# Performance work log

Measured on AMD Instinct MI355X. Metric: run time of the kernel, lower is better.

## Reference

```python
import jax, jax.numpy as jnp
import numpy as np

D_MODEL = 1024
NUM_HEADS = 16
D_KEY = D_MODEL // NUM_HEADS


def setup_inputs() -> dict:
    key = jax.random.key(0)
    ks = jax.random.split(key, 9)
    s = 1.0 / np.sqrt(D_MODEL)
    inp = {
        "x": jax.random.normal(ks[0], (4, 2048, D_MODEL), dtype=jnp.float32),
        "Wq": jax.random.uniform(ks[1], (D_MODEL, D_MODEL), jnp.float32, -s, s),
        "bq": jax.random.uniform(ks[2], (D_MODEL,), jnp.float32, -s, s),
        "Wk": jax.random.uniform(ks[3], (D_MODEL, D_MODEL), jnp.float32, -s, s),
        "bk": jax.random.uniform(ks[4], (D_MODEL,), jnp.float32, -s, s),
        "Wv": jax.random.uniform(ks[5], (D_MODEL, D_MODEL), jnp.float32, -s, s),
        "bv": jax.random.uniform(ks[6], (D_MODEL,), jnp.float32, -s, s),
        "Wo": jax.random.uniform(ks[7], (D_MODEL, D_MODEL), jnp.float32, -s, s),
        "bo": jax.random.uniform(ks[8], (D_MODEL,), jnp.float32, -s, s),
    }
    return inp


def reference(x, Wq, bq, Wk, bk, Wv, bv, Wo, bo):
    B, S, D = x.shape
    H, Dk = NUM_HEADS, D_KEY
    # QKV projections (torch Linear: x @ W.T + b; here W stored as [in,out])
    q = (x @ Wq + bq).reshape(B, S, H, Dk).transpose(0, 2, 1, 3)  # [B,H,S,Dk]
    k = (x @ Wk + bk).reshape(B, S, H, Dk).transpose(0, 2, 1, 3)
    v = (x @ Wv + bv).reshape(B, S, H, Dk).transpose(0, 2, 1, 3)
    logits = jnp.einsum("bhqd,bhkd->bhqk", q, k) / jnp.sqrt(jnp.float32(Dk))
    causal = jnp.triu(jnp.ones((S, S), dtype=bool), k=1)  # True above diagonal
    logits = jnp.where(causal, -jnp.inf, logits)
    attn = jax.nn.softmax(logits, axis=-1)
    out = jnp.einsum("bhqk,bhkd->bhqd", attn, v)  # [B,H,S,Dk]
    out = out.transpose(0, 2, 1, 3).reshape(B, S, D)
    return out @ Wo + bo
```

## Files before the change

### kernel.cpp

```cpp
#include <hip/hip_runtime.h>
#include <hip/hip_bf16.h>

#define DEVI __device__ __forceinline__

typedef __attribute__((ext_vector_type(8))) __bf16 bf16x8;
typedef __attribute__((ext_vector_type(4))) float f32x4;
typedef __attribute__((ext_vector_type(16))) float f32x16;
typedef __attribute__((ext_vector_type(8))) unsigned short ushort8;
typedef __attribute__((ext_vector_type(4))) int i32x4;

constexpr int D_MODEL = 1024;
constexpr int NHEAD   = 16;
constexpr int SEQ     = 2048;
constexpr int BATCH   = 4;
constexpr int MTOK    = BATCH * SEQ;

DEVI unsigned short f2bf(float x) {
  __hip_bfloat16 h = __float2bfloat16(x);
  return __builtin_bit_cast(unsigned short, h);
}

DEVI bf16x8 ld_bf8(const unsigned short* p) {
  ushort8 u = *reinterpret_cast<const ushort8*>(p);
  return __builtin_bit_cast(bf16x8, u);
}

DEVI void gload_lds16(const void* g, void* l) {
  __builtin_amdgcn_global_load_lds(
      (const __attribute__((address_space(1))) void*)g,
      (__attribute__((address_space(3))) void*)l, 16, 0, 0);
}

DEVI int cvtpk(float a, float b) {
  int r;
  asm("v_cvt_pk_bf16_f32 %0, %1, %2" : "=v"(r) : "v"(a), "v"(b));
  return r;
}
DEVI void pswap(int& a, int& b) {
  asm volatile("v_permlane32_swap_b32 %0, %1" : "+v"(a), "+v"(b));
}
DEVI float xhalf_sum(float x) { return x + __shfl_xor(x, 32, 64); }

DEVI float tree16sum(const float* p) {
  float a = p[0] + p[1], b = p[2] + p[3], c = p[4] + p[5], d = p[6] + p[7];
  float e = p[8] + p[9], f = p[10] + p[11], g = p[12] + p[13], h = p[14] + p[15];
  a += b; c += d; e += f; g += h;
  return (a + c) + (e + g);
}
DEVI bf16x8 mk_frag(const float* p, int off) {
  int w0 = cvtpk(p[off + 0], p[off + 1]);
  int w1 = cvtpk(p[off + 2], p[off + 3]);
  int w2 = cvtpk(p[off + 4], p[off + 5]);
  int w3 = cvtpk(p[off + 6], p[off + 7]);
  pswap(w0, w2);
  pswap(w1, w3);
  i32x4 v{w0, w1, w2, w3};
  return __builtin_bit_cast(bf16x8, v);
}

__global__ void cvt_f32_bf16(const float* __restrict__ in,
                             unsigned short* __restrict__ out, int n) {
  int i = (blockIdx.x * blockDim.x + threadIdx.x) * 4;
  if (i >= n) return;
  float4 v = *reinterpret_cast<const float4*>(in + i);
  ushort4 o;
  o.x = f2bf(v.x); o.y = f2bf(v.y); o.z = f2bf(v.z); o.w = f2bf(v.w);
  *reinterpret_cast<ushort4*>(out + i) = o;
}

__global__ void wt_kernel(const float* __restrict__ Wq, const float* __restrict__ Wk,
                          const float* __restrict__ Wv, const float* __restrict__ Wo,
                          unsigned short* __restrict__ Wtq, unsigned short* __restrict__ Wtk,
                          unsigned short* __restrict__ Wtv, unsigned short* __restrict__ Wto) {
  __shared__ float tile[64][65];
  const int wsel = blockIdx.z;
  const float* W = wsel == 0 ? Wq : wsel == 1 ? Wk : wsel == 2 ? Wv : Wo;
  unsigned short* Wt = wsel == 0 ? Wtq : wsel == 1 ? Wtk : wsel == 2 ? Wtv : Wto;
  const int k0 = blockIdx.x * 64, n0 = blockIdx.y * 64;
  const int tx = threadIdx.x & 63, ty = threadIdx.x >> 6;
  for (int r = ty; r < 64; r += 4)
    tile[r][tx] = W[(size_t)(k0 + r) * D_MODEL + n0 + tx];
  __syncthreads();
  for (int r = ty; r < 64; r += 4)
    Wt[(size_t)(n0 + r) * D_MODEL + k0 + tx] = f2bf(tile[tx][r]);
}

__global__ __launch_bounds__(256) void gemm128(
    const unsigned short* __restrict__ A,
    const unsigned short* __restrict__ Bt,
    const float* __restrict__ bias,
    void* __restrict__ outp, int mode, float scale) {
  constexpr int K = 1024, N = 1024;
  __shared__ __align__(16) unsigned short As[128 * 64];
  __shared__ __align__(16) unsigned short Bs[128 * 64];
  const int t = threadIdx.x;
  const int w = t >> 6, l = t & 63;
  const int bm = blockIdx.x >> 3, bn = blockIdx.x & 7;
  const int m0 = bm * 128, n0 = bn * 128;
  const int wm = (w >> 1) * 64, wn = (w & 1) * 64;
  const int lr = l & 15, lg = l >> 4;

  f32x4 acc[4][4] = {};

  for (int kt = 0; kt < K / 64; ++kt) {
    const int k0 = kt * 64;
    __syncthreads();
#pragma unroll
    for (int p = 0; p < 4; ++p) {
      const int seg = p * 4 + w;
      const int row = seg * 8 + (l >> 3);
      const int c = (l & 7) ^ (row & 7);
      gload_lds16(A + (size_t)(m0 + row) * K + k0 + c * 8, As + seg * 512);
      gload_lds16(Bt + (size_t)(n0 + row) * K + k0 + c * 8, Bs + seg * 512);
    }
    __syncthreads();
#pragma unroll
    for (int ks = 0; ks < 2; ++ks) {
      bf16x8 af[4], bfr[4];
      const int kk = lg + ks * 4;
#pragma unroll
      for (int i = 0; i < 4; ++i) {
        const int rowA = wm + i * 16 + lr;
        af[i] = ld_bf8(&As[rowA * 64 + ((kk ^ (rowA & 7)) * 8)]);
        const int rowB = wn + i * 16 + lr;
        bfr[i] = ld_bf8(&Bs[rowB * 64 + ((kk ^ (rowB & 7)) * 8)]);
      }
#pragma unroll
      for (int mi = 0; mi < 4; ++mi)
#pragma unroll
        for (int ni = 0; ni < 4; ++ni)
          acc[mi][ni] = __builtin_amdgcn_mfma_f32_16x16x32_bf16(
              af[mi], bfr[ni], acc[mi][ni], 0, 0, 0);
    }
  }

#pragma unroll
  for (int ni = 0; ni < 4; ++ni) {
    const int n = n0 + wn + ni * 16 + lr;
    const float bv = bias[n];
#pragma unroll
    for (int mi = 0; mi < 4; ++mi) {
#pragma unroll
      for (int r = 0; r < 4; ++r) {
        const int m = m0 + wm + mi * 16 + lg * 4 + r;
        const float v = (acc[mi][ni][r] + bv) * scale;
        if (mode == 2) {
          ((float*)outp)[(size_t)m * N + n] = v;
        } else {
          const int b = m >> 11, s = m & 2047, h = n >> 6, dk = n & 63;
          unsigned short* o = (unsigned short*)outp;
          if (mode == 0)
            o[(((size_t)(b * NHEAD + h) * SEQ + s) << 6) + dk] = f2bf(v);
          else
            o[(((size_t)(b * NHEAD + h) << 6) + dk) * SEQ + s] = f2bf(v);
        }
      }
    }
  }
}

__global__ __launch_bounds__(256) void attn_kernel(
    const unsigned short* __restrict__ Q,
    const unsigned short* __restrict__ Kt,
    const unsigned short* __restrict__ Vt,
    unsigned short* __restrict__ Oa) {
  __shared__ __align__(16) unsigned short Ks[2][64 * 64];
  __shared__ __align__(16) unsigned short Vs[2][64 * 64];
  const int t = threadIdx.x, w = t >> 6, l = t & 63;
  const int bid = blockIdx.x;
  const int tix = bid >> 6;
  const int tk = tix >> 2, tg = tix & 3;
  const int qt = tk == 0 ? 15 - tg : tk == 1 ? 8 + tg : tk == 2 ? 4 + tg : 3 - tg;
  const int bh = bid & 63;
  const int l31 = l & 31, hi = l >> 5;
  const int jcnt = 2 * qt + 2;
  const int q0w = qt * 128 + w * 32;
  const int qg = q0w + l31;

  const unsigned short* Qb = Q + ((size_t)bh * SEQ + qg) * 64;
  bf16x8 qf[4];
#pragma unroll
  for (int ks = 0; ks < 4; ++ks)
    qf[ks] = ld_bf8(Qb + ks * 16 + hi * 8);

  f32x16 psum = {};
  f32x16 oacc[2] = {};

  auto stage = [&](int jtile, int buf) {
#pragma unroll
    for (int i = 0; i < 2; ++i) {
      const int seg = w * 2 + i;
      const int row = seg * 8 + (l >> 3);
      const int cg = (l & 7) ^ (row & 7);
      gload_lds16(Kt + (((size_t)bh * SEQ + jtile * 64 + row) << 6) + cg * 8,
                  &Ks[buf][seg * 512]);
      gload_lds16(Vt + ((size_t)bh * 64 + row) * SEQ + jtile * 64 + cg * 8,
                  &Vs[buf][seg * 512]);
    }
  };

  stage(0, 0);
  __syncthreads();

  for (int jt = 0; jt < jcnt; ++jt) {
    const int cur = jt & 1;
    if (jt + 1 < jcnt) stage(jt + 1, cur ^ 1);
    const int j0 = jt * 64;
    const bool active = (j0 <= q0w + 31);
    if (active) {
      const bool live1 = (j0 < q0w);
      const bool maskT = (j0 + 32 >= q0w);

      f32x16 s0 = {}, s1 = {};
      __builtin_amdgcn_s_setprio(1);
#pragma unroll
      for (int ks = 0; ks < 4; ++ks) {
        bf16x8 kf = ld_bf8(&Ks[cur][l31 * 64 + ((((ks << 1) | hi) ^ (l31 & 7)) << 3)]);
        s0 = __builtin_amdgcn_mfma_f32_32x32x16_bf16(kf, qf[ks], s0, 0, 0, 0);
      }
      if (live1) {
#pragma unroll
        for (int ks = 0; ks < 4; ++ks) {
          const int r1 = 32 + l31;
          bf16x8 kf = ld_bf8(&Ks[cur][r1 * 64 + ((((ks << 1) | hi) ^ (r1 & 7)) << 3)]);
          s1 = __builtin_amdgcn_mfma_f32_32x32x16_bf16(kf, qf[ks], s1, 0, 0, 0);
        }
      }
      __builtin_amdgcn_s_setprio(0);

      float p0[16];
      if (maskT) {
#pragma unroll
        for (int r = 0; r < 16; ++r) {
          const int key = j0 + (r & 3) + ((r >> 2) << 3) + (hi << 2);
          p0[r] = (key > qg) ? 0.f : exp2f(s0[r]);
        }
      } else {
#pragma unroll
        for (int r = 0; r < 16; ++r) p0[r] = exp2f(s0[r]);
      }
#pragma unroll
      for (int r = 0; r < 16; ++r) psum[r] += p0[r];

      __builtin_amdgcn_s_setprio(1);
#pragma unroll
      for (int ks = 0; ks < 2; ++ks) {
        bf16x8 pf = mk_frag(p0, ks * 8);
#pragma unroll
        for (int dt = 0; dt < 2; ++dt) {
          const int rv = dt * 32 + l31;
          bf16x8 vf = ld_bf8(&Vs[cur][rv * 64 + ((((ks << 1) | hi) ^ (rv & 7)) << 3)]);
          oacc[dt] = __builtin_amdgcn_mfma_f32_32x32x16_bf16(vf, pf, oacc[dt], 0, 0, 0);
        }
      }
      __builtin_amdgcn_s_setprio(0);

      if (live1) {
        float p1[16];
        if (maskT) {
#pragma unroll
          for (int r = 0; r < 16; ++r) {
            const int key = j0 + 32 + (r & 3) + ((r >> 2) << 3) + (hi << 2);
            p1[r] = (key > qg) ? 0.f : exp2f(s1[r]);
          }
        } else {
#pragma unroll
          for (int r = 0; r < 16; ++r) p1[r] = exp2f(s1[r]);
        }
#pragma unroll
        for (int r = 0; r < 16; ++r) psum[r] += p1[r];
        __builtin_amdgcn_s_setprio(1);
#pragma unroll
        for (int ks = 0; ks < 2; ++ks) {
          bf16x8 pf = mk_frag(p1, ks * 8);
#pragma unroll
          for (int dt = 0; dt < 2; ++dt) {
            const int rv = dt * 32 + l31;
            bf16x8 vf = ld_bf8(&Vs[cur][rv * 64 + (((((ks + 2) << 1) | hi) ^ (rv & 7)) << 3)]);
            oacc[dt] = __builtin_amdgcn_mfma_f32_32x32x16_bf16(vf, pf, oacc[dt], 0, 0, 0);
          }
        }
        __builtin_amdgcn_s_setprio(0);
      }
    }
    __syncthreads();
  }

  float pa[16];
#pragma unroll
  for (int r = 0; r < 16; ++r) pa[r] = psum[r];
  const float l_ = xhalf_sum(tree16sum(pa));
  const float rinv = 1.f / l_;
  const int b = bh >> 4, h = bh & 15;
  unsigned short* orow = Oa + ((size_t)(b * SEQ) + qg) * D_MODEL + h * 64;
#pragma unroll
  for (int dt = 0; dt < 2; ++dt)
#pragma unroll
    for (int g = 0; g < 4; ++g) {
      const int d = dt * 32 + g * 8 + hi * 4;
      uint2 u;
      u.x = (unsigned)cvtpk(oacc[dt][g * 4 + 0] * rinv, oacc[dt][g * 4 + 1] * rinv);
      u.y = (unsigned)cvtpk(oacc[dt][g * 4 + 2] * rinv, oacc[dt][g * 4 + 3] * rinv);
      *reinterpret_cast<uint2*>(orow + d) = u;
    }
}

extern "C" void kernel_launch(void* const* d_in, const int* in_sizes, int n_in,
                              void* d_out, int out_size, void* d_ws, size_t ws_size,
                              hipStream_t stream) {
  const float* x  = (const float*)d_in[0];
  const float* Wq = (const float*)d_in[1];
  const float* bq = (const float*)d_in[2];
  const float* Wk = (const float*)d_in[3];
  const float* bk = (const float*)d_in[4];
  const float* Wv = (const float*)d_in[5];
  const float* bv = (const float*)d_in[6];
  const float* Wo = (const float*)d_in[7];
  const float* bo = (const float*)d_in[8];

  char* ws = (char*)d_ws;
  unsigned short* xb    = (unsigned short*)(ws + 0);
  unsigned short* attnb = (unsigned short*)(ws + 0);
  unsigned short* wtq   = (unsigned short*)(ws + 16777216);
  unsigned short* wtk   = (unsigned short*)(ws + 18874368);
  unsigned short* wtv   = (unsigned short*)(ws + 20971520);
  unsigned short* wto   = (unsigned short*)(ws + 23068672);
  unsigned short* Qw    = (unsigned short*)(ws + 25165824);
  unsigned short* Kw    = (unsigned short*)(ws + 41943040);
  unsigned short* Vtw   = (unsigned short*)(ws + 58720256);

  cvt_f32_bf16<<<8192, 256, 0, stream>>>(x, xb, MTOK * D_MODEL);
  wt_kernel<<<dim3(16, 16, 4), 256, 0, stream>>>(Wq, Wk, Wv, Wo, wtq, wtk, wtv, wto);

  gemm128<<<512, 256, 0, stream>>>(xb, wtq, bq, (void*)Qw, 0, 0.18033688011112042f);
  gemm128<<<512, 256, 0, stream>>>(xb, wtk, bk, (void*)Kw, 0, 1.0f);
  gemm128<<<512, 256, 0, stream>>>(xb, wtv, bv, (void*)Vtw, 1, 1.0f);

  attn_kernel<<<1024, 256, 0, stream>>>(Qw, Kw, Vtw, attnb);

  gemm128<<<512, 256, 0, stream>>>(attnb, wto, bo, d_out, 2, 1.0f);
}
```

Baseline: 210.5 us.

## Compute softmax row sums via MFMA with ones vector and precompute LDS offsets

Replaces the per-element VALU accumulation of exp values and the final cross-lane tree reduction with an extra MFMA that multiplies a ones fragment by the bf16 probability fragment. Precomputes swizzled LDS offsets and global staging pointers for the attention kernel to cut address arithmetic. It also remaps GEMM block indices so consecutive blocks walk along M for a fixed N tile, changing cache reuse. The row sum now uses bf16-rounded probabilities, which matches the numerator, at the cost of extra MFMA work per tile.

```diff
diff --git a/kernel.cpp b/kernel.cpp
--- a/kernel.cpp
+++ b/kernel.cpp
@@ -38,14 +38,6 @@
 }
 DEVI void pswap(int& a, int& b) {
   asm volatile("v_permlane32_swap_b32 %0, %1" : "+v"(a), "+v"(b));
-}
-DEVI float xhalf_sum(float x) { return x + __shfl_xor(x, 32, 64); }
-
-DEVI float tree16sum(const float* p) {
-  float a = p[0] + p[1], b = p[2] + p[3], c = p[4] + p[5], d = p[6] + p[7];
-  float e = p[8] + p[9], f = p[10] + p[11], g = p[12] + p[13], h = p[14] + p[15];
-  a += b; c += d; e += f; g += h;
-  return (a + c) + (e + g);
 }
 DEVI bf16x8 mk_frag(const float* p, int off) {
   int w0 = cvtpk(p[off + 0], p[off + 1]);
@@ -95,7 +87,8 @@
   __shared__ __align__(16) unsigned short Bs[128 * 64];
   const int t = threadIdx.x;
   const int w = t >> 6, l = t & 63;
-  const int bm = blockIdx.x >> 3, bn = blockIdx.x & 7;
+  const int bid2 = ((blockIdx.x & 7) << 6) | (blockIdx.x >> 3);
+  const int bm = bid2 >> 3, bn = bid2 & 7;
   const int m0 = bm * 128, n0 = bn * 128;
   const int wm = (w >> 1) * 64, wn = (w & 1) * 64;
   const int lr = l & 15, lg = l >> 4;
@@ -164,8 +157,8 @@
     const unsigned short* __restrict__ Kt,
     const unsigned short* __restrict__ Vt,
     unsigned short* __restrict__ Oa) {
-  __shared__ __align__(16) unsigned short Ks[2][64 * 64];
-  __shared__ __align__(16) unsigned short Vs[2][64 * 64];
+  __shared__ __align__(16) unsigned short Ks[2 * 4096];
+  __shared__ __align__(16) unsigned short Vs[2 * 4096];
   const int t = threadIdx.x, w = t >> 6, l = t & 63;
   const int bid = blockIdx.x;
   const int tix = bid >> 6;
@@ -183,28 +176,43 @@
   for (int ks = 0; ks < 4; ++ks)
     qf[ks] = ld_bf8(Qb + ks * 16 + hi * 8);
 
-  f32x16 psum = {};
+  int kbase[4];
+#pragma unroll
+  for (int ks = 0; ks < 4; ++ks)
+    kbase[ks] = l31 * 64 + ((((ks << 1) | hi) ^ (l31 & 7)) << 3);
+
+  const i32x4 onesv{0x3F803F80, 0x3F803F80, 0x3F803F80, 0x3F803F80};
+  const bf16x8 ones = __builtin_bit_cast(bf16x8, onesv);
+
+  f32x16 accl = {};
   f32x16 oacc[2] = {};
 
+  const int seg0 = w * 2, srow0 = seg0 * 8 + (l >> 3);
+  const int seg1 = seg0 + 1, srow1 = seg1 * 8 + (l >> 3);
+  const int cg0 = (l & 7) ^ (srow0 & 7), cg1 = (l & 7) ^ (srow1 & 7);
+  const unsigned short* gK0 = Kt + (((size_t)bh * SEQ + srow0) << 6) + cg0 * 8;
+  const unsigned short* gK1 = Kt + (((size_t)bh * SEQ + srow1) << 6) + cg1 * 8;
+  const unsigned short* gV0 = Vt + ((size_t)bh * 64 + srow0) * SEQ + cg0 * 8;
+  const unsigned short* gV1 = Vt + ((size_t)bh * 64 + srow1) * SEQ + cg1 * 8;
+  unsigned short* lK0 = Ks + seg0 * 512;
+  unsigned short* lK1 = Ks + seg1 * 512;
+  unsigned short* lV0 = Vs + seg0 * 512;
+  unsigned short* lV1 = Vs + seg1 * 512;
+
   auto stage = [&](int jtile, int buf) {
-#pragma unroll
-    for (int i = 0; i < 2; ++i) {
-      const int seg = w * 2 + i;
-      const int row = seg * 8 + (l >> 3);
-      const int cg = (l & 7) ^ (row & 7);
-      gload_lds16(Kt + (((size_t)bh * SEQ + jtile * 64 + row) << 6) + cg * 8,
-                  &Ks[buf][seg * 512]);
-      gload_lds16(Vt + ((size_t)bh * 64 + row) * SEQ + jtile * 64 + cg * 8,
-                  &Vs[buf][seg * 512]);
-    }
+    const int bo = buf << 12;
+    gload_lds16(gK0 + (size_t)jtile * 4096, lK0 + bo);
+    gload_lds16(gK1 + (size_t)jtile * 4096, lK1 + bo);
+    gload_lds16(gV0 + (size_t)jtile * 64, lV0 + bo);
+    gload_lds16(gV1 + (size_t)jtile * 64, lV1 + bo);
   };
 
   stage(0, 0);
   __syncthreads();
 
   for (int jt = 0; jt < jcnt; ++jt) {
-    const int cur = jt & 1;
-    if (jt + 1 < jcnt) stage(jt + 1, cur ^ 1);
+    const int co = (jt & 1) << 12;
+    if (jt + 1 < jcnt) stage(jt + 1, (jt & 1) ^ 1);
     const int j0 = jt * 64;
     const bool active = (j0 <= q0w + 31);
     if (active) {
@@ -215,20 +223,19 @@
       __builtin_amdgcn_s_setprio(1);
 #pragma unroll
       for (int ks = 0; ks < 4; ++ks) {
-        bf16x8 kf = ld_bf8(&Ks[cur][l31 * 64 + ((((ks << 1) | hi) ^ (l31 & 7)) << 3)]);
+        bf16x8 kf = ld_bf8(&Ks[co + kbase[ks]]);
         s0 = __builtin_amdgcn_mfma_f32_32x32x16_bf16(kf, qf[ks], s0, 0, 0, 0);
       }
       if (live1) {
 #pragma unroll
         for (int ks = 0; ks < 4; ++ks) {
-          const int r1 = 32 + l31;
-          bf16x8 kf = ld_bf8(&Ks[cur][r1 * 64 + ((((ks << 1) | hi) ^ (r1 & 7)) << 3)]);
+          bf16x8 kf = ld_bf8(&Ks[co + kbase[ks] + 2048]);
           s1 = __builtin_amdgcn_mfma_f32_32x32x16_bf16(kf, qf[ks], s1, 0, 0, 0);
         }
       }
       __builtin_amdgcn_s_setprio(0);
 
-      float p0[16];
+      float p0[16], p1[16];
       if (maskT) {
 #pragma unroll
         for (int r = 0; r < 16; ++r) {
@@ -239,24 +246,7 @@
 #pragma unroll
         for (int r = 0; r < 16; ++r) p0[r] = exp2f(s0[r]);
       }
-#pragma unroll
-      for (int r = 0; r < 16; ++r) psum[r] += p0[r];
-
-      __builtin_amdgcn_s_setprio(1);
-#pragma unroll
-      for (int ks = 0; ks < 2; ++ks) {
-        bf16x8 pf = mk_frag(p0, ks * 8);
-#pragma unroll
-        for (int dt = 0; dt < 2; ++dt) {
-          const int rv = dt * 32 + l31;
-          bf16x8 vf = ld_bf8(&Vs[cur][rv * 64 + ((((ks << 1) | hi) ^ (rv & 7)) << 3)]);
-          oacc[dt] = __builtin_amdgcn_mfma_f32_32x32x16_bf16(vf, pf, oacc[dt], 0, 0, 0);
-        }
-      }
-      __builtin_amdgcn_s_setprio(0);
-
       if (live1) {
-        float p1[16];
         if (maskT) {
 #pragma unroll
           for (int r = 0; r < 16; ++r) {
@@ -267,30 +257,37 @@
 #pragma unroll
           for (int r = 0; r < 16; ++r) p1[r] = exp2f(s1[r]);
         }
-#pragma unroll
-        for (int r = 0; r < 16; ++r) psum[r] += p1[r];
-        __builtin_amdgcn_s_setprio(1);
+      }
+
+      __builtin_amdgcn_s_setprio(1);
+#pragma unroll
+      for (int ks = 0; ks < 2; ++ks) {
+        bf16x8 pf = mk_frag(p0, ks * 8);
+        accl = __builtin_amdgcn_mfma_f32_32x32x16_bf16(ones, pf, accl, 0, 0, 0);
+#pragma unroll
+        for (int dt = 0; dt < 2; ++dt) {
+          bf16x8 vf = ld_bf8(&Vs[co + kbase[ks] + dt * 2048]);
+          oacc[dt] = __builtin_amdgcn_mfma_f32_32x32x16_bf16(vf, pf, oacc[dt], 0, 0, 0);
+        }
+      }
+      if (live1) {
 #pragma unroll
         for (int ks = 0; ks < 2; ++ks) {
           bf16x8 pf = mk_frag(p1, ks * 8);
+          accl = __builtin_amdgcn_mfma_f32_32x32x16_bf16(ones, pf, accl, 0, 0, 0);
 #pragma unroll
           for (int dt = 0; dt < 2; ++dt) {
-            const int rv = dt * 32 + l31;
-            bf16x8 vf = ld_bf8(&Vs[cur][rv * 64 + (((((ks + 2) << 1) | hi) ^ (rv & 7)) << 3)]);
+            bf16x8 vf = ld_bf8(&Vs[co + (kbase[ks] ^ 32) + dt * 2048]);
             oacc[dt] = __builtin_amdgcn_mfma_f32_32x32x16_bf16(vf, pf, oacc[dt], 0, 0, 0);
           }
         }
-        __builtin_amdgcn_s_setprio(0);
-      }
+      }
+      __builtin_amdgcn_s_setprio(0);
     }
     __syncthreads();
   }
 
-  float pa[16];
-#pragma unroll
-  for (int r = 0; r < 16; ++r) pa[r] = psum[r];
-  const float l_ = xhalf_sum(tree16sum(pa));
-  const float rinv = 1.f / l_;
+  const float rinv = 1.f / accl[0];
   const int b = bh >> 4, h = bh & 15;
   unsigned short* orow = Oa + ((size_t)(b * SEQ) + qg) * D_MODEL + h * 64;
 #pragma unroll
```

New measurement: 212.3 us. About the same (+0.9%).

## Fuse Q/K/V projection GEMMs into one launch with XCD-aware block mapping

Applied to the files above, without the earlier changes.

Replaces three separate projection GEMM launches with a single kernel covering a concatenated 3072-column weight (the transposed Wq, Wk, Wv buffers are contiguous in workspace), choosing bias, scale and output layout per block. Block indices are remapped so blocks sharing the same A row tile land on the same XCD, improving L2 reuse; the output GEMM gets the same remap and a simplified epilogue. This removes launch gaps and tail underutilization between the GEMMs, but relies on the weight buffers being adjacent in memory.

```diff
diff --git a/kernel.cpp b/kernel.cpp
--- a/kernel.cpp
+++ b/kernel.cpp
@@ -85,17 +85,96 @@
     Wt[(size_t)(n0 + r) * D_MODEL + k0 + tx] = f2bf(tile[tx][r]);
 }
 
-__global__ __launch_bounds__(256) void gemm128(
+__global__ __launch_bounds__(256) void gemm_qkv(
+    const unsigned short* __restrict__ A,
+    const unsigned short* __restrict__ Bt,
+    const float* __restrict__ bq, const float* __restrict__ bk,
+    const float* __restrict__ bv,
+    unsigned short* __restrict__ Qw, unsigned short* __restrict__ Kw,
+    unsigned short* __restrict__ Vtw, float qscale) {
+  constexpr int K = 1024;
+  __shared__ __align__(16) unsigned short As[128 * 64];
+  __shared__ __align__(16) unsigned short Bs[128 * 64];
+  const int t = threadIdx.x;
+  const int w = t >> 6, l = t & 63;
+  const int xcd = blockIdx.x & 7, ci = blockIdx.x >> 3;
+  const int bm = xcd * 8 + ci / 24, bn = ci % 24;
+  const int m0 = bm * 128, n0g = bn * 128;
+  const int wm = (w >> 1) * 64, wn = (w & 1) * 64;
+  const int lr = l & 15, lg = l >> 4;
+
+  f32x4 acc[4][4] = {};
+
+  for (int kt = 0; kt < K / 64; ++kt) {
+    const int k0 = kt * 64;
+    __syncthreads();
+#pragma unroll
+    for (int p = 0; p < 4; ++p) {
+      const int seg = p * 4 + w;
+      const int row = seg * 8 + (l >> 3);
+      const int c = (l & 7) ^ (row & 7);
+      gload_lds16(A + (size_t)(m0 + row) * K + k0 + c * 8, As + seg * 512);
+      gload_lds16(Bt + (size_t)(n0g + row) * K + k0 + c * 8, Bs + seg * 512);
+    }
+    __syncthreads();
+#pragma unroll
+    for (int ks = 0; ks < 2; ++ks) {
+      bf16x8 af[4], bfr[4];
+      const int kk = lg + ks * 4;
+#pragma unroll
+      for (int i = 0; i < 4; ++i) {
+        const int rowA = wm + i * 16 + lr;
+        af[i] = ld_bf8(&As[rowA * 64 + ((kk ^ (rowA & 7)) * 8)]);
+        const int rowB = wn + i * 16 + lr;
+        bfr[i] = ld_bf8(&Bs[rowB * 64 + ((kk ^ (rowB & 7)) * 8)]);
+      }
+#pragma unroll
+      for (int mi = 0; mi < 4; ++mi)
+#pragma unroll
+        for (int ni = 0; ni < 4; ++ni)
+          acc[mi][ni] = __builtin_amdgcn_mfma_f32_16x16x32_bf16(
+              af[mi], bfr[ni], acc[mi][ni], 0, 0, 0);
+    }
+  }
+
+  const int sel = bn >> 3;
+  const float* bias = sel == 0 ? bq : sel == 1 ? bk : bv;
+  const float scale = sel == 0 ? qscale : 1.f;
+  unsigned short* o = sel == 0 ? Qw : sel == 1 ? Kw : Vtw;
+  const int nl0 = n0g & 1023;
+#pragma unroll
+  for (int ni = 0; ni < 4; ++ni) {
+    const int n = nl0 + wn + ni * 16 + lr;
+    const float bvv = bias[n];
+    const int h = n >> 6, dk = n & 63;
+#pragma unroll
+    for (int mi = 0; mi < 4; ++mi) {
+#pragma unroll
+      for (int r = 0; r < 4; ++r) {
+        const int m = m0 + wm + mi * 16 + lg * 4 + r;
+        const float v = (acc[mi][ni][r] + bvv) * scale;
+        const int b = m >> 11, s = m & 2047;
+        if (sel < 2)
+          o[(((size_t)(b * NHEAD + h) * SEQ + s) << 6) + dk] = f2bf(v);
+        else
+          o[(((size_t)(b * NHEAD + h) << 6) + dk) * SEQ + s] = f2bf(v);
+      }
+    }
+  }
+}
+
+__global__ __launch_bounds__(256) void gemm_o(
     const unsigned short* __restrict__ A,
     const unsigned short* __restrict__ Bt,
     const float* __restrict__ bias,
-    void* __restrict__ outp, int mode, float scale) {
+    float* __restrict__ outp) {
   constexpr int K = 1024, N = 1024;
   __shared__ __align__(16) unsigned short As[128 * 64];
   __shared__ __align__(16) unsigned short Bs[128 * 64];
   const int t = threadIdx.x;
   const int w = t >> 6, l = t & 63;
-  const int bm = blockIdx.x >> 3, bn = blockIdx.x & 7;
+  const int bid2 = ((blockIdx.x & 7) << 6) | (blockIdx.x >> 3);
+  const int bm = bid2 >> 3, bn = bid2 & 7;
   const int m0 = bm * 128, n0 = bn * 128;
   const int wm = (w >> 1) * 64, wn = (w & 1) * 64;
   const int lr = l & 15, lg = l >> 4;
@@ -143,17 +222,7 @@
 #pragma unroll
       for (int r = 0; r < 4; ++r) {
         const int m = m0 + wm + mi * 16 + lg * 4 + r;
-        const float v = (acc[mi][ni][r] + bv) * scale;
-        if (mode == 2) {
-          ((float*)outp)[(size_t)m * N + n] = v;
-        } else {
-          const int b = m >> 11, s = m & 2047, h = n >> 6, dk = n & 63;
-          unsigned short* o = (unsigned short*)outp;
-          if (mode == 0)
-            o[(((size_t)(b * NHEAD + h) * SEQ + s) << 6) + dk] = f2bf(v);
-          else
-            o[(((size_t)(b * NHEAD + h) << 6) + dk) * SEQ + s] = f2bf(v);
-        }
+        outp[(size_t)m * N + n] = acc[mi][ni][r] + bv;
       }
     }
   }
@@ -332,11 +401,10 @@
   cvt_f32_bf16<<<8192, 256, 0, stream>>>(x, xb, MTOK * D_MODEL);
   wt_kernel<<<dim3(16, 16, 4), 256, 0, stream>>>(Wq, Wk, Wv, Wo, wtq, wtk, wtv, wto);
 
-  gemm128<<<512, 256, 0, stream>>>(xb, wtq, bq, (void*)Qw, 0, 0.18033688011112042f);
-  gemm128<<<512, 256, 0, stream>>>(xb, wtk, bk, (void*)Kw, 0, 1.0f);
-  gemm128<<<512, 256, 0, stream>>>(xb, wtv, bv, (void*)Vtw, 1, 1.0f);
+  gemm_qkv<<<1536, 256, 0, stream>>>(xb, wtq, bq, bk, bv, Qw, Kw, Vtw,
+                                     0.18033688011112042f);
 
   attn_kernel<<<1024, 256, 0, stream>>>(Qw, Kw, Vtw, attnb);
 
-  gemm128<<<512, 256, 0, stream>>>(attnb, wto, bo, d_out, 2, 1.0f);
-}
+  gemm_o<<<512, 256, 0, stream>>>(attnb, wto, bo, (float*)d_out);
+}
```

After: 202.9 us. 1.04x faster.
